# Kernel tuning notes

Hardware: AMD Instinct MI355X
Metric: run time of the kernel (lower is better)

Reference implementation:

```python
import jax, jax.numpy as jnp
import numpy as np

N_NODES = 100000
N_EDGES = 3200000
N_GRAPHS = 64
IN_DIM = 64
LATENT = 64
DIST_STD = 1.0


def _gcn_conv(x, W, b, src, dst, dinv):
    """PyG GCNConv: out = D^-1/2 (A+I) D^-1/2 (x W) + b, with dinv = deg^-1/2."""
    n = x.shape[0]
    h = x @ W  # [N, out]
    coef = dinv[src] * dinv[dst]  # per-edge norm
    agg = jax.ops.segment_sum(h[src] * coef[:, None], dst, num_segments=n)
    # self-loop contribution with norm dinv[i]^2
    return agg + h * (dinv * dinv)[:, None] + b


def _mean_pool(x, batch, num_graphs):
    sums = jax.ops.segment_sum(x, batch, num_segments=num_graphs)
    cnts = jax.ops.segment_sum(jnp.ones((x.shape[0],), x.dtype), batch, num_segments=num_graphs)
    return sums / jnp.maximum(cnts, 1.0)[:, None]


def setup_inputs() -> dict:
    key = jax.random.key(0)
    ks = jax.random.split(key, 12)
    x = jax.random.normal(ks[0], (N_NODES, IN_DIM), jnp.float32)
    edge_index = jax.random.randint(ks[1], (2, N_EDGES), 0, N_NODES, jnp.int64 if jax.config.jax_enable_x64 else jnp.int32).astype(jnp.int32)
    batch = jnp.sort(jax.random.randint(ks[2], (N_NODES,), 0, N_GRAPHS)).astype(jnp.int32)

    def glorot(k, shape):
        fan_in, fan_out = shape
        s = jnp.sqrt(6.0 / (fan_in + fan_out))
        return jax.random.uniform(k, shape, jnp.float32, -s, s)

    return {
        "x": x, "edge_index": edge_index, "batch": batch,
        "W1m": glorot(ks[3], (IN_DIM, 16)), "b1m": jnp.zeros((16,), jnp.float32),
        "W2m": glorot(ks[4], (16, 32)), "b2m": jnp.zeros((32,), jnp.float32),
        "W3m": glorot(ks[5], (32, LATENT)), "b3m": jnp.zeros((LATENT,), jnp.float32),
        "W1l": glorot(ks[6], (IN_DIM, 16)), "b1l": jnp.zeros((16,), jnp.float32),
        "W2l": glorot(ks[7], (16, 32)), "b2l": jnp.zeros((32,), jnp.float32),
        "W3l": glorot(ks[8], (32, LATENT)), "b3l": jnp.zeros((LATENT,), jnp.float32),
        "Wfc": glorot(ks[9], (LATENT, 160000)), "bfc": jnp.zeros((160000,), jnp.float32),
        "eps": jax.random.normal(ks[10], (N_GRAPHS, LATENT), jnp.float32) * DIST_STD,
    }


def reference(x, edge_index, batch, W1m, b1m, W2m, b2m, W3m, b3m,
              W1l, b1l, W2l, b2l, W3l, b3l, Wfc, bfc, eps):
    src, dst = edge_index[0], edge_index[1]
    n = x.shape[0]
    # degrees include self-loop (+1)
    deg = jax.ops.segment_sum(jnp.ones((src.shape[0],), x.dtype), dst, num_segments=n) + 1.0
    dinv = jax.lax.rsqrt(deg)

    mu = jax.nn.relu(_gcn_conv(x, W1m, b1m, src, dst, dinv))
    mu = jax.nn.relu(_gcn_conv(mu, W2m, b2m, src, dst, dinv))
    mu = jax.nn.relu(_gcn_conv(mu, W3m, b3m, src, dst, dinv))
    mu = _mean_pool(mu, batch, N_GRAPHS)

    log = jax.nn.relu(_gcn_conv(x, W1l, b1l, src, dst, dinv))
    log = jax.nn.relu(_gcn_conv(log, W2l, b2l, src, dst, dinv))
    log = jax.nn.relu(_gcn_conv(log, W3l, b3l, src, dst, dinv))
    logvar = _mean_pool(log, batch, N_GRAPHS)

    # latent sample (training mode): z = mu + eps * exp(0.5*logvar)
    z = mu + eps * jnp.exp(0.5 * logvar)

    # decode: sigmoid(z Wfc + bfc) -> [G, 400, 400]
    output = jax.nn.sigmoid(z @ Wfc + bfc).reshape(-1, 400, 400)
    return output, mu, logvar
```

## Files before the change

kernel.cpp:

```cpp
#include <hip/hip_runtime.h>
#include <hip/hip_bf16.h>

#define N_NODES 100000
#define N_EDGES 3200000
#define N_GRAPHS 64
#define NB 391
#define KCH 8192
#define NCHUNK ((N_EDGES + KCH - 1) / KCH)
#define MAXBKT 10240
#define NBLK3 (N_NODES / 32)

__device__ __forceinline__ void atomAddF(float* p, float v) {
    unsafeAtomicAdd(p, v);
}

__device__ __forceinline__ float lo2f(unsigned u) { return __uint_as_float(u << 16); }
__device__ __forceinline__ float hi2f(unsigned u) { return __uint_as_float(u & 0xFFFF0000u); }
__device__ __forceinline__ unsigned pack2(float a, float b) {
    unsigned ha = __bfloat16_as_ushort(__float2bfloat16(a));
    unsigned hb = __bfloat16_as_ushort(__float2bfloat16(b));
    return ha | (hb << 16);
}

__global__ __launch_bounds__(512) void k_binCount(const int* __restrict__ dst,
                                                  int* __restrict__ gcount) {
    __shared__ int hist[NB];
    for (int t = threadIdx.x; t < NB; t += 512) hist[t] = 0;
    __syncthreads();
    int base = blockIdx.x * KCH;
    int cnt = min(KCH, N_EDGES - base);
    for (int i = threadIdx.x; i < cnt; i += 512)
        atomicAdd(&hist[dst[base + i] >> 8], 1);
    __syncthreads();
    for (int t = threadIdx.x; t < NB; t += 512)
        if (hist[t]) atomicAdd(&gcount[t], hist[t]);
}

__global__ __launch_bounds__(512) void k_scanB(const int* __restrict__ gcount,
                                               int* __restrict__ gbase,
                                               int* __restrict__ gcursor,
                                               int* __restrict__ rowptr) {
    __shared__ int s[512];
    int v = (threadIdx.x < NB) ? gcount[threadIdx.x] : 0;
    s[threadIdx.x] = v;
    __syncthreads();
    for (int off = 1; off < 512; off <<= 1) {
        int t = (threadIdx.x >= off) ? s[threadIdx.x - off] : 0;
        __syncthreads();
        s[threadIdx.x] += t;
        __syncthreads();
    }
    if (threadIdx.x < NB) {
        int e = s[threadIdx.x] - v;
        gbase[threadIdx.x] = e;
        gcursor[threadIdx.x] = e;
    }
    if (threadIdx.x == 0) rowptr[N_NODES] = N_EDGES;
}

__global__ __launch_bounds__(512) void k_binA(const int* __restrict__ src,
                                              const int* __restrict__ dst,
                                              int* __restrict__ gcursor,
                                              int* __restrict__ binned) {
    __shared__ int hist[512];
    __shared__ int sc[512];
    __shared__ int sexc[512];
    __shared__ int rbase[512];
    __shared__ int stage[KCH];
    hist[threadIdx.x] = 0;
    __syncthreads();
    int base = blockIdx.x * KCH;
    int cnt = min(KCH, N_EDGES - base);
    int myb[16], mypos[16];
    int nmine = 0;
    for (int i = 0; i < 16; ++i) {
        int idx = i * 512 + threadIdx.x;
        if (idx < cnt) {
            int b = dst[base + idx] >> 8;
            myb[nmine] = b;
            mypos[nmine] = atomicAdd(&hist[b], 1);
            ++nmine;
        }
    }
    __syncthreads();
    int v = hist[threadIdx.x];
    sc[threadIdx.x] = v;
    __syncthreads();
    for (int off = 1; off < 512; off <<= 1) {
        int t = (threadIdx.x >= off) ? sc[threadIdx.x - off] : 0;
        __syncthreads();
        sc[threadIdx.x] += t;
        __syncthreads();
    }
    sexc[threadIdx.x] = sc[threadIdx.x] - v;
    __syncthreads();
    if (threadIdx.x < NB && v > 0)
        rbase[threadIdx.x] = atomicAdd(&gcursor[threadIdx.x], v);
    for (int k = 0; k < nmine; ++k) {
        int e = base + k * 512 + threadIdx.x;
        int p = ((dst[e] & 255) << 24) | src[e];
        stage[sexc[myb[k]] + mypos[k]] = p;
    }
    __syncthreads();
    for (int j = threadIdx.x; j < cnt; j += 512) {
        int lo = 0, hi = NB - 1;
        while (lo < hi) {
            int mid = (lo + hi + 1) >> 1;
            if (sexc[mid] <= j) lo = mid; else hi = mid - 1;
        }
        binned[rbase[lo] + (j - sexc[lo])] = stage[j];
    }
}

__global__ __launch_bounds__(512) void k_passB(const int* __restrict__ gbase,
                                               int* __restrict__ csr,
                                               int* __restrict__ rowptr,
                                               float* __restrict__ dinv) {
    int b = blockIdx.x;
    int rb = gbase[b];
    int re = (b == NB - 1) ? N_EDGES : gbase[b + 1];
    int cnt = re - rb;
    int nbase = b << 8;
    int nn = min(nbase + 256, N_NODES) - nbase;
    __shared__ int stage[MAXBKT];
    __shared__ int nhist[256];
    __shared__ int sc[256];
    __shared__ int ncur[256];
    for (int t = threadIdx.x; t < 256; t += 512) nhist[t] = 0;
    __syncthreads();
    for (int j = threadIdx.x; j < cnt; j += 512) {
        int p = csr[rb + j];
        stage[j] = p;
        atomicAdd(&nhist[((unsigned)p) >> 24], 1);
    }
    __syncthreads();
    if (threadIdx.x < 256) sc[threadIdx.x] = nhist[threadIdx.x];
    __syncthreads();
    for (int off = 1; off < 256; off <<= 1) {
        int t = (threadIdx.x < 256 && threadIdx.x >= off) ? sc[threadIdx.x - off] : 0;
        __syncthreads();
        if (threadIdx.x < 256) sc[threadIdx.x] += t;
        __syncthreads();
    }
    if (threadIdx.x < 256) {
        int e = sc[threadIdx.x] - nhist[threadIdx.x];
        ncur[threadIdx.x] = e;
        if (threadIdx.x < nn) {
            rowptr[nbase + threadIdx.x] = rb + e;
            dinv[nbase + threadIdx.x] = rsqrtf((float)nhist[threadIdx.x] + 1.0f);
        }
    }
    __syncthreads();
    for (int j = threadIdx.x; j < cnt; j += 512) {
        int p = stage[j];
        int slot = atomicAdd(&ncur[((unsigned)p) >> 24], 1);
        csr[rb + slot] = p;
    }
}

template<int LOGW, bool BIAS_RELU, bool OB, bool PRE>
__global__ void __launch_bounds__(256) k_gatherB(
        const int* __restrict__ rowptr, const int* __restrict__ csr,
        const unsigned* __restrict__ in ,
        const float* __restrict__ dinv,
        const float* __restrict__ ba, const float* __restrict__ bb,
        void* __restrict__ out) {
    constexpr int W8 = (1 << LOGW) / 8;
    constexpr int NPB = 256 / W8;
    int n = blockIdx.x * NPB + (threadIdx.x / W8);
    if (n >= N_NODES) return;
    int sub = threadIdx.x % W8;
    const uint4* in4 = (const uint4*)in;
    uint4 u = in4[(size_t)n * W8 + sub];
    float a0 = lo2f(u.x), a1 = hi2f(u.x), a2 = lo2f(u.y), a3 = hi2f(u.y);
    float a4 = lo2f(u.z), a5 = hi2f(u.z), a6 = lo2f(u.w), a7 = hi2f(u.w);
    int j = rowptr[n], end = rowptr[n + 1];
    for (; j + 8 <= end; j += 8) {
        int s0 = csr[j] & 0xFFFFFF;
        int s1 = csr[j + 1] & 0xFFFFFF;
        int s2 = csr[j + 2] & 0xFFFFFF;
        int s3 = csr[j + 3] & 0xFFFFFF;
        int s4 = csr[j + 4] & 0xFFFFFF;
        int s5 = csr[j + 5] & 0xFFFFFF;
        int s6 = csr[j + 6] & 0xFFFFFF;
        int s7 = csr[j + 7] & 0xFFFFFF;
        uint4 v0 = in4[(size_t)s0 * W8 + sub];
        uint4 v1 = in4[(size_t)s1 * W8 + sub];
        uint4 v2 = in4[(size_t)s2 * W8 + sub];
        uint4 v3 = in4[(size_t)s3 * W8 + sub];
        uint4 v4 = in4[(size_t)s4 * W8 + sub];
        uint4 v5 = in4[(size_t)s5 * W8 + sub];
        uint4 v6 = in4[(size_t)s6 * W8 + sub];
        uint4 v7 = in4[(size_t)s7 * W8 + sub];
        a0 += ((lo2f(v0.x) + lo2f(v1.x)) + (lo2f(v2.x) + lo2f(v3.x)))
            + ((lo2f(v4.x) + lo2f(v5.x)) + (lo2f(v6.x) + lo2f(v7.x)));
        a1 += ((hi2f(v0.x) + hi2f(v1.x)) + (hi2f(v2.x) + hi2f(v3.x)))
            + ((hi2f(v4.x) + hi2f(v5.x)) + (hi2f(v6.x) + hi2f(v7.x)));
        a2 += ((lo2f(v0.y) + lo2f(v1.y)) + (lo2f(v2.y) + lo2f(v3.y)))
            + ((lo2f(v4.y) + lo2f(v5.y)) + (lo2f(v6.y) + lo2f(v7.y)));
        a3 += ((hi2f(v0.y) + hi2f(v1.y)) + (hi2f(v2.y) + hi2f(v3.y)))
            + ((hi2f(v4.y) + hi2f(v5.y)) + (hi2f(v6.y) + hi2f(v7.y)));
        a4 += ((lo2f(v0.z) + lo2f(v1.z)) + (lo2f(v2.z) + lo2f(v3.z)))
            + ((lo2f(v4.z) + lo2f(v5.z)) + (lo2f(v6.z) + lo2f(v7.z)));
        a5 += ((hi2f(v0.z) + hi2f(v1.z)) + (hi2f(v2.z) + hi2f(v3.z)))
            + ((hi2f(v4.z) + hi2f(v5.z)) + (hi2f(v6.z) + hi2f(v7.z)));
        a6 += ((lo2f(v0.w) + lo2f(v1.w)) + (lo2f(v2.w) + lo2f(v3.w)))
            + ((lo2f(v4.w) + lo2f(v5.w)) + (lo2f(v6.w) + lo2f(v7.w)));
        a7 += ((hi2f(v0.w) + hi2f(v1.w)) + (hi2f(v2.w) + hi2f(v3.w)))
            + ((hi2f(v4.w) + hi2f(v5.w)) + (hi2f(v6.w) + hi2f(v7.w)));
    }
    for (; j < end; ++j) {
        int s = csr[j] & 0xFFFFFF;
        uint4 v = in4[(size_t)s * W8 + sub];
        a0 += lo2f(v.x); a1 += hi2f(v.x);
        a2 += lo2f(v.y); a3 += hi2f(v.y);
        a4 += lo2f(v.z); a5 += hi2f(v.z);
        a6 += lo2f(v.w); a7 += hi2f(v.w);
    }
    float di = dinv[n];
    a0 *= di; a1 *= di; a2 *= di; a3 *= di;
    a4 *= di; a5 *= di; a6 *= di; a7 *= di;
    if (BIAS_RELU) {
        constexpr int H = (1 << LOGW) / 2;
        int d = sub * 8;
        const float* bp = (d < H) ? (ba + d) : (bb + d - H);
        a0 = fmaxf(a0 + bp[0], 0.0f);
        a1 = fmaxf(a1 + bp[1], 0.0f);
        a2 = fmaxf(a2 + bp[2], 0.0f);
        a3 = fmaxf(a3 + bp[3], 0.0f);
        a4 = fmaxf(a4 + bp[4], 0.0f);
        a5 = fmaxf(a5 + bp[5], 0.0f);
        a6 = fmaxf(a6 + bp[6], 0.0f);
        a7 = fmaxf(a7 + bp[7], 0.0f);
    }
    if (PRE) {
        a0 *= di; a1 *= di; a2 *= di; a3 *= di;
        a4 *= di; a5 *= di; a6 *= di; a7 *= di;
    }
    if (OB) {
        ((uint4*)out)[(size_t)n * W8 + sub] =
            make_uint4(pack2(a0, a1), pack2(a2, a3), pack2(a4, a5), pack2(a6, a7));
    } else {
        constexpr int OUT4 = (1 << LOGW) / 4;
        float4* o4 = (float4*)out;
        o4[(size_t)n * OUT4 + sub * 2]     = make_float4(a0, a1, a2, a3);
        o4[(size_t)n * OUT4 + sub * 2 + 1] = make_float4(a4, a5, a6, a7);
    }
}

#define FMA4(A, W) \
    A.x = fmaf(r, W.x, A.x); A.y = fmaf(r, W.y, A.y); \
    A.z = fmaf(r, W.z, A.z); A.w = fmaf(r, W.w, A.w);

__global__ void __launch_bounds__(256) k_gd3(
        const int* __restrict__ rowptr, const int* __restrict__ csr,
        const unsigned* __restrict__ in,
        const float* __restrict__ dinv,
        const float* __restrict__ W3m, const float* __restrict__ b3m,
        const float* __restrict__ W3l, const float* __restrict__ b3l,
        const int* __restrict__ batch,
        float* __restrict__ part0, float* __restrict__ part1,
        int* __restrict__ pg0, int* __restrict__ pg1) {
    __shared__ float s_ali[32 * 160];
    __shared__ float agg[32 * 68];
    __shared__ float sbias[128];
    __shared__ int   sbatch[32];
    __shared__ int   ssplit;
    float* sWall = s_ali;
    float* h3s   = s_ali;

    for (int t = threadIdx.x; t < 4096; t += 256) {
        int k = t >> 7, D = t & 127;
        float wv = (D < 64) ? W3m[k * 64 + D] : W3l[k * 64 + (D - 64)];
        sWall[k * 160 + (D >> 4) * 20 + (D & 15)] = wv;
    }
    if (threadIdx.x < 128)
        sbias[threadIdx.x] = (threadIdx.x < 64) ? b3m[threadIdx.x]
                                                : b3l[threadIdx.x - 64];
    int nbase = blockIdx.x * 32;
    if (threadIdx.x < 32) sbatch[threadIdx.x] = batch[nbase + threadIdx.x];

    int ln  = threadIdx.x >> 3;
    int sub = threadIdx.x & 7;
    int n = nbase + ln;
    const uint4* in4 = (const uint4*)in;
    uint4 u = in4[(size_t)n * 8 + sub];
    float a0 = lo2f(u.x), a1 = hi2f(u.x), a2 = lo2f(u.y), a3 = hi2f(u.y);
    float a4 = lo2f(u.z), a5 = hi2f(u.z), a6 = lo2f(u.w), a7 = hi2f(u.w);
    int j = rowptr[n], end = rowptr[n + 1];
    for (; j + 8 <= end; j += 8) {
        int s0 = csr[j] & 0xFFFFFF;
        int s1 = csr[j + 1] & 0xFFFFFF;
        int s2 = csr[j + 2] & 0xFFFFFF;
        int s3 = csr[j + 3] & 0xFFFFFF;
        int s4 = csr[j + 4] & 0xFFFFFF;
        int s5 = csr[j + 5] & 0xFFFFFF;
        int s6 = csr[j + 6] & 0xFFFFFF;
        int s7 = csr[j + 7] & 0xFFFFFF;
        uint4 v0 = in4[(size_t)s0 * 8 + sub];
        uint4 v1 = in4[(size_t)s1 * 8 + sub];
        uint4 v2 = in4[(size_t)s2 * 8 + sub];
        uint4 v3 = in4[(size_t)s3 * 8 + sub];
        uint4 v4 = in4[(size_t)s4 * 8 + sub];
        uint4 v5 = in4[(size_t)s5 * 8 + sub];
        uint4 v6 = in4[(size_t)s6 * 8 + sub];
        uint4 v7 = in4[(size_t)s7 * 8 + sub];
        a0 += ((lo2f(v0.x) + lo2f(v1.x)) + (lo2f(v2.x) + lo2f(v3.x)))
            + ((lo2f(v4.x) + lo2f(v5.x)) + (lo2f(v6.x) + lo2f(v7.x)));
        a1 += ((hi2f(v0.x) + hi2f(v1.x)) + (hi2f(v2.x) + hi2f(v3.x)))
            + ((hi2f(v4.x) + hi2f(v5.x)) + (hi2f(v6.x) + hi2f(v7.x)));
        a2 += ((lo2f(v0.y) + lo2f(v1.y)) + (lo2f(v2.y) + lo2f(v3.y)))
            + ((lo2f(v4.y) + lo2f(v5.y)) + (lo2f(v6.y) + lo2f(v7.y)));
        a3 += ((hi2f(v0.y) + hi2f(v1.y)) + (hi2f(v2.y) + hi2f(v3.y)))
            + ((hi2f(v4.y) + hi2f(v5.y)) + (hi2f(v6.y) + hi2f(v7.y)));
        a4 += ((lo2f(v0.z) + lo2f(v1.z)) + (lo2f(v2.z) + lo2f(v3.z)))
            + ((lo2f(v4.z) + lo2f(v5.z)) + (lo2f(v6.z) + lo2f(v7.z)));
        a5 += ((hi2f(v0.z) + hi2f(v1.z)) + (hi2f(v2.z) + hi2f(v3.z)))
            + ((hi2f(v4.z) + hi2f(v5.z)) + (hi2f(v6.z) + hi2f(v7.z)));
        a6 += ((lo2f(v0.w) + lo2f(v1.w)) + (lo2f(v2.w) + lo2f(v3.w)))
            + ((lo2f(v4.w) + lo2f(v5.w)) + (lo2f(v6.w) + lo2f(v7.w)));
        a7 += ((hi2f(v0.w) + hi2f(v1.w)) + (hi2f(v2.w) + hi2f(v3.w)))
            + ((hi2f(v4.w) + hi2f(v5.w)) + (hi2f(v6.w) + hi2f(v7.w)));
    }
    for (; j < end; ++j) {
        int s = csr[j] & 0xFFFFFF;
        uint4 v = in4[(size_t)s * 8 + sub];
        a0 += lo2f(v.x); a1 += hi2f(v.x);
        a2 += lo2f(v.y); a3 += hi2f(v.y);
        a4 += lo2f(v.z); a5 += hi2f(v.z);
        a6 += lo2f(v.w); a7 += hi2f(v.w);
    }
    float di = dinv[n];
    a0 *= di; a1 *= di; a2 *= di; a3 *= di;
    a4 *= di; a5 *= di; a6 *= di; a7 *= di;
    {
        float* ap = &agg[ln * 68 + sub * 8];
        *(float4*)&ap[0] = make_float4(a0, a1, a2, a3);
        *(float4*)&ap[4] = make_float4(a4, a5, a6, a7);
    }
    if (threadIdx.x == 0) {
        int sp = 32;
        int ga = sbatch[0];
        for (int i = 1; i < 32; ++i)
            if (sbatch[i] != ga) { sp = i; break; }
        ssplit = sp;
    }
    __syncthreads();

    int ln2 = threadIdx.x >> 3;
    int q   = threadIdx.x & 7;
    int Dbase = q * 16;
    int koff = (q >= 4) ? 32 : 0;
    float4 c0 = *(const float4*)&sbias[Dbase];
    float4 c1 = *(const float4*)&sbias[Dbase + 4];
    float4 c2 = *(const float4*)&sbias[Dbase + 8];
    float4 c3 = *(const float4*)&sbias[Dbase + 12];
    const float* ag = &agg[ln2 * 68 + koff];
    const float* wq = &sWall[q * 20];
    #pragma unroll
    for (int k = 0; k < 32; ++k) {
        float r = ag[k];
        const float* wr = &wq[k * 160];
        float4 w0 = *(const float4*)&wr[0];
        float4 w1 = *(const float4*)&wr[4];
        float4 w2 = *(const float4*)&wr[8];
        float4 w3 = *(const float4*)&wr[12];
        FMA4(c0, w0)
        FMA4(c1, w1)
        FMA4(c2, w2)
        FMA4(c3, w3)
    }
    c0.x = fmaxf(c0.x, 0.f); c0.y = fmaxf(c0.y, 0.f);
    c0.z = fmaxf(c0.z, 0.f); c0.w = fmaxf(c0.w, 0.f);
    c1.x = fmaxf(c1.x, 0.f); c1.y = fmaxf(c1.y, 0.f);
    c1.z = fmaxf(c1.z, 0.f); c1.w = fmaxf(c1.w, 0.f);
    c2.x = fmaxf(c2.x, 0.f); c2.y = fmaxf(c2.y, 0.f);
    c2.z = fmaxf(c2.z, 0.f); c2.w = fmaxf(c2.w, 0.f);
    c3.x = fmaxf(c3.x, 0.f); c3.y = fmaxf(c3.y, 0.f);
    c3.z = fmaxf(c3.z, 0.f); c3.w = fmaxf(c3.w, 0.f);
    __syncthreads();

    {
        float* hp = &h3s[ln2 * 132 + Dbase];
        *(float4*)&hp[0]  = c0;
        *(float4*)&hp[4]  = c1;
        *(float4*)&hp[8]  = c2;
        *(float4*)&hp[12] = c3;
    }
    __syncthreads();
    {
        int d    = threadIdx.x & 127;
        int slot = threadIdx.x >> 7;
        int sp = ssplit;
        int s = slot ? sp : 0;
        int e = slot ? 32 : sp;
        float acc = 0.f;
        for (int nn = s; nn < e; ++nn)
            acc += h3s[nn * 132 + d];
        int b = blockIdx.x;
        if (slot == 0) {
            part0[(size_t)b * 128 + d] = acc;
            if (d == 0) pg0[b] = sbatch[0];
        } else {
            part1[(size_t)b * 128 + d] = acc;
            if (d == 0) pg1[b] = (sp < 32) ? sbatch[31] : -1;
        }
    }
}

__global__ void __launch_bounds__(128) k_poolR(
        const float* __restrict__ part0, const float* __restrict__ part1,
        const int* __restrict__ pg0, const int* __restrict__ pg1,
        const int* __restrict__ batch, float* __restrict__ pool) {
    int g = blockIdx.x;
    __shared__ int sb[2];
    if (threadIdx.x < 2) {
        int target = g + threadIdx.x;
        int lo = 0, hi = N_NODES;
        while (lo < hi) {
            int mid = (lo + hi) >> 1;
            if (batch[mid] < target) lo = mid + 1; else hi = mid;
        }
        sb[threadIdx.x] = lo;
    }
    __syncthreads();
    int ns = sb[0], ne = sb[1];
    int d = threadIdx.x;
    float acc = 0.f;
    if (ne > ns) {
        int b0 = ns >> 5, b1 = (ne - 1) >> 5;
        for (int b = b0; b <= b1; ++b) {
            if (pg0[b] == g) acc += part0[(size_t)b * 128 + d];
            if (pg1[b] == g) acc += part1[(size_t)b * 128 + d];
        }
    }
    pool[g * 128 + d] = acc;
}

template<int IN_W, int OUT_HALF, int A_OFF, int A_W, int B_OFF, bool BR, bool OB, bool DS>
__global__ void k_dense4(const float* __restrict__ in,
                         const float* __restrict__ Wa, const float* __restrict__ ba,
                         const float* __restrict__ Wb, const float* __restrict__ bb,
                         const float* __restrict__ dinv,
                         void* __restrict__ out) {
    __shared__ float sWa[A_W * OUT_HALF];
    __shared__ float sWb[A_W * OUT_HALF];
    __shared__ float sba[OUT_HALF];
    __shared__ float sbb[OUT_HALF];
    for (int t = threadIdx.x; t < A_W * OUT_HALF; t += 256) {
        sWa[t] = Wa[t];
        sWb[t] = Wb[t];
    }
    if (BR && threadIdx.x < OUT_HALF) {
        sba[threadIdx.x] = ba[threadIdx.x];
        sbb[threadIdx.x] = bb[threadIdx.x];
    }
    __syncthreads();
    constexpr int TPN = OUT_HALF / 2;
    int idx = blockIdx.x * 256 + threadIdx.x;
    int n = idx / TPN;
    int q = idx % TPN;
    bool isB = (q * 4) >= OUT_HALF;
    int dd = q * 4 - (isB ? OUT_HALF : 0);
    const float* sW = isB ? sWb : sWa;
    int ko = isB ? B_OFF : A_OFF;
    float4 acc;
    if (BR) {
        const float* bp = isB ? (sbb + dd) : (sba + dd);
        acc = make_float4(bp[0], bp[1], bp[2], bp[3]);
    } else {
        acc = make_float4(0.f, 0.f, 0.f, 0.f);
    }
    const float* row = in + (size_t)n * IN_W + ko;
    #pragma unroll
    for (int k = 0; k < A_W; ++k) {
        float r = row[k];
        float4 wv = *(const float4*)&sW[k * OUT_HALF + dd];
        acc.x = fmaf(r, wv.x, acc.x);
        acc.y = fmaf(r, wv.y, acc.y);
        acc.z = fmaf(r, wv.z, acc.z);
        acc.w = fmaf(r, wv.w, acc.w);
    }
    if (BR) {
        acc.x = fmaxf(acc.x, 0.f); acc.y = fmaxf(acc.y, 0.f);
        acc.z = fmaxf(acc.z, 0.f); acc.w = fmaxf(acc.w, 0.f);
    }
    if (DS) {
        float dn = dinv[n];
        acc.x *= dn; acc.y *= dn; acc.z *= dn; acc.w *= dn;
    }
    if (OB) {
        ((uint2*)out)[idx] = make_uint2(pack2(acc.x, acc.y), pack2(acc.z, acc.w));
    } else {
        ((float4*)out)[idx] = acc;
    }
}

__global__ void k_final(const float* __restrict__ pool, const int* __restrict__ batch,
                        const float* __restrict__ eps, float* __restrict__ zbuf,
                        float* __restrict__ out_mu, float* __restrict__ out_lv) {
    __shared__ int sb[5];
    int g0 = blockIdx.x * 4;
    if (threadIdx.x < 5) {
        int target = g0 + threadIdx.x;
        int lo = 0, hi = N_NODES;
        if (target >= N_GRAPHS) {
            lo = N_NODES;
        } else {
            while (lo < hi) {
                int mid = (lo + hi) >> 1;
                if (batch[mid] < target) lo = mid + 1; else hi = mid;
            }
        }
        sb[threadIdx.x] = lo;
    }
    __syncthreads();
    int idx = blockIdx.x * 256 + threadIdx.x;
    int g = idx >> 6;
    int k = idx & 63;
    int gl = threadIdx.x >> 6;
    float c = fmaxf((float)(sb[gl + 1] - sb[gl]), 1.0f);
    float mu = pool[g * 128 + k] / c;
    float lv = pool[g * 128 + 64 + k] / c;
    zbuf[k * 64 + g] = mu + eps[idx] * __expf(0.5f * lv);
    out_mu[idx] = mu;
    out_lv[idx] = lv;
}

__global__ void __launch_bounds__(256) k_decode(const float* __restrict__ zT,
                                                const float* __restrict__ Wfc,
                                                const float* __restrict__ bfc,
                                                float* __restrict__ out) {
    int j = (blockIdx.x >> 1) * 256 + threadIdx.x;
    int gh = (blockIdx.x & 1) * 32;
    const float* zp = zT + gh;
    float bias = bfc[j];
    float acc[32];
    #pragma unroll
    for (int g = 0; g < 32; ++g) acc[g] = bias;
    #pragma unroll 8
    for (int k = 0; k < 64; ++k) {
        float w = Wfc[(size_t)k * 160000 + j];
        #pragma unroll
        for (int g = 0; g < 32; ++g)
            acc[g] = fmaf(zp[k * 64 + g], w, acc[g]);
    }
    #pragma unroll
    for (int g = 0; g < 32; ++g) {
        float s = 1.0f / (1.0f + __expf(-acc[g]));
        out[(size_t)(gh + g) * 160000 + j] = s;
    }
}

extern "C" void kernel_launch(void* const* d_in, const int* in_sizes, int n_in,
                              void* d_out, int out_size, void* d_ws, size_t ws_size,
                              hipStream_t stream) {
    const float* x     = (const float*)d_in[0];
    const int*   ei    = (const int*)d_in[1];
    const int*   batch = (const int*)d_in[2];
    const float *W1m = (const float*)d_in[3],  *b1m = (const float*)d_in[4];
    const float *W2m = (const float*)d_in[5],  *b2m = (const float*)d_in[6];
    const float *W3m = (const float*)d_in[7],  *b3m = (const float*)d_in[8];
    const float *W1l = (const float*)d_in[9],  *b1l = (const float*)d_in[10];
    const float *W2l = (const float*)d_in[11], *b2l = (const float*)d_in[12];
    const float *W3l = (const float*)d_in[13], *b3l = (const float*)d_in[14];
    const float *Wfc = (const float*)d_in[15], *bfc = (const float*)d_in[16];
    const float *eps = (const float*)d_in[17];

    const int* srcv = ei;
    const int* dstv = ei + N_EDGES;

    char* w = (char*)d_ws;
    auto alloc = [&](size_t bytes) -> char* {
        char* p = w;
        w += (bytes + 255) & ~(size_t)255;
        return p;
    };
    int*   gcount = (int*)  alloc((size_t)NB * 4);
    int*   gbase  = (int*)  alloc((size_t)NB * 4);
    int*   gcursor= (int*)  alloc((size_t)NB * 4);
    int*   rowptr = (int*)  alloc((size_t)(N_NODES + 1) * 4);
    float* dinv   = (float*)alloc((size_t)N_NODES * 4);
    float* pool   = (float*)alloc((size_t)N_GRAPHS * 128 * 4);
    float* zbuf   = (float*)alloc((size_t)N_GRAPHS * 64 * 4);
    float* arena = (float*)alloc((size_t)N_NODES * 192 * 4);
    float* A   = arena;
    float* B   = arena + (size_t)N_NODES * 64;
    int*   csr = (int*)(arena + (size_t)N_NODES * 128);
    float* part0 = A;
    float* part1 = A + (size_t)NBLK3 * 128;
    int*   pg0   = (int*)(A + (size_t)2 * NBLK3 * 128);
    int*   pg1   = pg0 + NBLK3;

    float* out    = (float*)d_out;
    float* out_mu = out + 10240000;
    float* out_lv = out + 10240000 + 4096;

    hipMemsetAsync(gcount, 0, (size_t)NB * 4, stream);

    k_binCount<<<NCHUNK, 512, 0, stream>>>(dstv, gcount);
    k_scanB<<<1, 512, 0, stream>>>(gcount, gbase, gcursor, rowptr);
    k_binA<<<NCHUNK, 512, 0, stream>>>(srcv, dstv, gcursor, csr);
    k_passB<<<NB, 512, 0, stream>>>(gbase, csr, rowptr, dinv);

    k_dense4<64, 16, 0, 64, 0, false, true, true><<<N_NODES * 8 / 256, 256, 0, stream>>>(
        x, W1m, b1m, W1l, b1l, dinv, A);
    k_gatherB<5, true, true, true><<<(N_NODES + 63) / 64, 256, 0, stream>>>(
        rowptr, csr, (const unsigned*)A, dinv, b1m, b1l, B);

    k_gatherB<5, false, false, false><<<(N_NODES + 63) / 64, 256, 0, stream>>>(
        rowptr, csr, (const unsigned*)B, dinv, b1m, b1l, A);
    k_dense4<32, 32, 0, 16, 16, true, true, true><<<N_NODES * 16 / 256, 256, 0, stream>>>(
        A, W2m, b2m, W2l, b2l, dinv, B);

    k_gd3<<<NBLK3, 256, 0, stream>>>(
        rowptr, csr, (const unsigned*)B, dinv, W3m, b3m, W3l, b3l, batch,
        part0, part1, pg0, pg1);
    k_poolR<<<N_GRAPHS, 128, 0, stream>>>(part0, part1, pg0, pg1, batch, pool);

    k_final<<<16, 256, 0, stream>>>(pool, batch, eps, zbuf, out_mu, out_lv);

    k_decode<<<1250, 256, 0, stream>>>(zbuf, Wfc, bfc, out);
}
```

Baseline: 450.0 us.

## Scatter binned edges directly, fuse pooling with finalize, split gd3 launch

The binning kernel now packs each edge in registers and writes it straight to its global bucket slot. This removes the shared-memory prefix scan, the staging buffer and the per-element binary search, at the cost of less coalesced global writes. The pooling reduction is fused with the mean/reparameterization step, which drops the k_final kernel and the pool buffer round trip. The k_gd3 launch is also split into two half-size launches through a block offset, which adds a launch without any clear benefit.

After: 463.6 us. +3.0%, slower.

```diff
diff --git a/kernel.cpp b/kernel.cpp
--- a/kernel.cpp
+++ b/kernel.cpp
@@ -63,52 +63,39 @@
                                               int* __restrict__ gcursor,
                                               int* __restrict__ binned) {
     __shared__ int hist[512];
-    __shared__ int sc[512];
-    __shared__ int sexc[512];
     __shared__ int rbase[512];
-    __shared__ int stage[KCH];
     hist[threadIdx.x] = 0;
     __syncthreads();
     int base = blockIdx.x * KCH;
     int cnt = min(KCH, N_EDGES - base);
-    int myb[16], mypos[16];
-    int nmine = 0;
+    int pk[16];
+    int meta[16];
+    #pragma unroll
     for (int i = 0; i < 16; ++i) {
         int idx = i * 512 + threadIdx.x;
         if (idx < cnt) {
-            int b = dst[base + idx] >> 8;
-            myb[nmine] = b;
-            mypos[nmine] = atomicAdd(&hist[b], 1);
-            ++nmine;
+            int d = dst[base + idx];
+            int b = d >> 8;
+            int pos = atomicAdd(&hist[b], 1);
+            pk[i] = ((d & 255) << 24) | src[base + idx];
+            meta[i] = (b << 13) | pos;
+        } else {
+            meta[i] = -1;
         }
     }
     __syncthreads();
-    int v = hist[threadIdx.x];
-    sc[threadIdx.x] = v;
-    __syncthreads();
-    for (int off = 1; off < 512; off <<= 1) {
-        int t = (threadIdx.x >= off) ? sc[threadIdx.x - off] : 0;
-        __syncthreads();
-        sc[threadIdx.x] += t;
-        __syncthreads();
-    }
-    sexc[threadIdx.x] = sc[threadIdx.x] - v;
-    __syncthreads();
-    if (threadIdx.x < NB && v > 0)
-        rbase[threadIdx.x] = atomicAdd(&gcursor[threadIdx.x], v);
-    for (int k = 0; k < nmine; ++k) {
-        int e = base + k * 512 + threadIdx.x;
-        int p = ((dst[e] & 255) << 24) | src[e];
-        stage[sexc[myb[k]] + mypos[k]] = p;
-    }
-    __syncthreads();
-    for (int j = threadIdx.x; j < cnt; j += 512) {
-        int lo = 0, hi = NB - 1;
-        while (lo < hi) {
-            int mid = (lo + hi + 1) >> 1;
-            if (sexc[mid] <= j) lo = mid; else hi = mid - 1;
+    if (threadIdx.x < NB) {
+        int v = hist[threadIdx.x];
+        if (v > 0) rbase[threadIdx.x] = atomicAdd(&gcursor[threadIdx.x], v);
+    }
+    __syncthreads();
+    #pragma unroll
+    for (int i = 0; i < 16; ++i) {
+        if (meta[i] >= 0) {
+            int b = meta[i] >> 13;
+            int pos = meta[i] & 8191;
+            binned[rbase[b] + pos] = pk[i];
         }
-        binned[rbase[lo] + (j - sexc[lo])] = stage[j];
     }
 }
 
@@ -260,7 +247,7 @@
         const float* __restrict__ W3l, const float* __restrict__ b3l,
         const int* __restrict__ batch,
         float* __restrict__ part0, float* __restrict__ part1,
-        int* __restrict__ pg0, int* __restrict__ pg1) {
+        int* __restrict__ pg0, int* __restrict__ pg1, int boff) {
     __shared__ float s_ali[32 * 160];
     __shared__ float agg[32 * 68];
     __shared__ float sbias[128];
@@ -269,6 +256,7 @@
     float* sWall = s_ali;
     float* h3s   = s_ali;
 
+    int blk = blockIdx.x + boff;
     for (int t = threadIdx.x; t < 4096; t += 256) {
         int k = t >> 7, D = t & 127;
         float wv = (D < 64) ? W3m[k * 64 + D] : W3l[k * 64 + (D - 64)];
@@ -277,7 +265,7 @@
     if (threadIdx.x < 128)
         sbias[threadIdx.x] = (threadIdx.x < 64) ? b3m[threadIdx.x]
                                                 : b3l[threadIdx.x - 64];
-    int nbase = blockIdx.x * 32;
+    int nbase = blk * 32;
     if (threadIdx.x < 32) sbatch[threadIdx.x] = batch[nbase + threadIdx.x];
 
     int ln  = threadIdx.x >> 3;
@@ -397,23 +385,25 @@
         float acc = 0.f;
         for (int nn = s; nn < e; ++nn)
             acc += h3s[nn * 132 + d];
-        int b = blockIdx.x;
         if (slot == 0) {
-            part0[(size_t)b * 128 + d] = acc;
-            if (d == 0) pg0[b] = sbatch[0];
+            part0[(size_t)blk * 128 + d] = acc;
+            if (d == 0) pg0[blk] = sbatch[0];
         } else {
-            part1[(size_t)b * 128 + d] = acc;
-            if (d == 0) pg1[b] = (sp < 32) ? sbatch[31] : -1;
+            part1[(size_t)blk * 128 + d] = acc;
+            if (d == 0) pg1[blk] = (sp < 32) ? sbatch[31] : -1;
         }
     }
 }
 
-__global__ void __launch_bounds__(128) k_poolR(
+__global__ void __launch_bounds__(128) k_poolF(
         const float* __restrict__ part0, const float* __restrict__ part1,
         const int* __restrict__ pg0, const int* __restrict__ pg1,
-        const int* __restrict__ batch, float* __restrict__ pool) {
+        const int* __restrict__ batch, const float* __restrict__ eps,
+        float* __restrict__ zbuf, float* __restrict__ out_mu,
+        float* __restrict__ out_lv) {
     int g = blockIdx.x;
     __shared__ int sb[2];
+    __shared__ float spool[128];
     if (threadIdx.x < 2) {
         int target = g + threadIdx.x;
         int lo = 0, hi = N_NODES;
@@ -434,7 +424,17 @@
             if (pg1[b] == g) acc += part1[(size_t)b * 128 + d];
         }
     }
-    pool[g * 128 + d] = acc;
+    spool[d] = acc;
+    __syncthreads();
+    if (threadIdx.x < 64) {
+        int k = threadIdx.x;
+        float c = fmaxf((float)(ne - ns), 1.0f);
+        float mu = spool[k] / c;
+        float lv = spool[64 + k] / c;
+        zbuf[k * 64 + g] = mu + eps[g * 64 + k] * __expf(0.5f * lv);
+        out_mu[g * 64 + k] = mu;
+        out_lv[g * 64 + k] = lv;
+    }
 }
 
 template<int IN_W, int OUT_HALF, int A_OFF, int A_W, int B_OFF, bool BR, bool OB, bool DS>
@@ -494,37 +494,6 @@
     } else {
         ((float4*)out)[idx] = acc;
     }
-}
-
-__global__ void k_final(const float* __restrict__ pool, const int* __restrict__ batch,
-                        const float* __restrict__ eps, float* __restrict__ zbuf,
-                        float* __restrict__ out_mu, float* __restrict__ out_lv) {
-    __shared__ int sb[5];
-    int g0 = blockIdx.x * 4;
-    if (threadIdx.x < 5) {
-        int target = g0 + threadIdx.x;
-        int lo = 0, hi = N_NODES;
-        if (target >= N_GRAPHS) {
-            lo = N_NODES;
-        } else {
-            while (lo < hi) {
-                int mid = (lo + hi) >> 1;
-                if (batch[mid] < target) lo = mid + 1; else hi = mid;
-            }
-        }
-        sb[threadIdx.x] = lo;
-    }
-    __syncthreads();
-    int idx = blockIdx.x * 256 + threadIdx.x;
-    int g = idx >> 6;
-    int k = idx & 63;
-    int gl = threadIdx.x >> 6;
-    float c = fmaxf((float)(sb[gl + 1] - sb[gl]), 1.0f);
-    float mu = pool[g * 128 + k] / c;
-    float lv = pool[g * 128 + 64 + k] / c;
-    zbuf[k * 64 + g] = mu + eps[idx] * __expf(0.5f * lv);
-    out_mu[idx] = mu;
-    out_lv[idx] = lv;
 }
 
 __global__ void __launch_bounds__(256) k_decode(const float* __restrict__ zT,
@@ -581,7 +550,6 @@
     int*   gcursor= (int*)  alloc((size_t)NB * 4);
     int*   rowptr = (int*)  alloc((size_t)(N_NODES + 1) * 4);
     float* dinv   = (float*)alloc((size_t)N_NODES * 4);
-    float* pool   = (float*)alloc((size_t)N_GRAPHS * 128 * 4);
     float* zbuf   = (float*)alloc((size_t)N_GRAPHS * 64 * 4);
     float* arena = (float*)alloc((size_t)N_NODES * 192 * 4);
     float* A   = arena;
@@ -613,12 +581,15 @@
     k_dense4<32, 32, 0, 16, 16, true, true, true><<<N_NODES * 16 / 256, 256, 0, stream>>>(
         A, W2m, b2m, W2l, b2l, dinv, B);
 
-    k_gd3<<<NBLK3, 256, 0, stream>>>(
+    k_gd3<<<NBLK3 / 2, 256, 0, stream>>>(
         rowptr, csr, (const unsigned*)B, dinv, W3m, b3m, W3l, b3l, batch,
-        part0, part1, pg0, pg1);
-    k_poolR<<<N_GRAPHS, 128, 0, stream>>>(part0, part1, pg0, pg1, batch, pool);
-
-    k_final<<<16, 256, 0, stream>>>(pool, batch, eps, zbuf, out_mu, out_lv);
+        part0, part1, pg0, pg1, 0);
+    k_gd3<<<NBLK3 - NBLK3 / 2, 256, 0, stream>>>(
+        rowptr, csr, (const unsigned*)B, dinv, W3m, b3m, W3l, b3l, batch,
+        part0, part1, pg0, pg1, NBLK3 / 2);
+
+    k_poolF<<<N_GRAPHS, 128, 0, stream>>>(part0, part1, pg0, pg1, batch, eps,
+                                          zbuf, out_mu, out_lv);
 
     k_decode<<<1250, 256, 0, stream>>>(zbuf, Wfc, bfc, out);
 }
```
